# Kernel optimization log

Measured on AMD Instinct MI355X. Metric: run time of the kernel, lower is better.

Reference implementation:

```python
import jax, jax.numpy as jnp
import numpy as np

B, T, E, H = 4, 1024, 1024, 16
D = E // H  # head_dim = 64


def setup_inputs() -> dict:
    key = jax.random.key(0)
    ks = jax.random.split(key, 6)
    s = 0.02  # realistic init scale for stable softmax
    return {
        "hidden_states": jax.random.normal(ks[0], (B, T, E), jnp.float32),
        "attention_mask": jnp.zeros((B, 1, T, T), jnp.float32),
        "Wq": jax.random.normal(ks[1], (E, E), jnp.float32) * s,
        "bq": jnp.zeros((E,), jnp.float32),
        "Wk": jax.random.normal(ks[2], (E, E), jnp.float32) * s,
        "bk": jnp.zeros((E,), jnp.float32),
        "Wv": jax.random.normal(ks[3], (E, E), jnp.float32) * s,
        "bv": jnp.zeros((E,), jnp.float32),
        "Wo": jax.random.normal(ks[4], (E, E), jnp.float32) * s,
        "bo": jnp.zeros((E,), jnp.float32),
    }


def reference(hidden_states, attention_mask, Wq, bq, Wk, bk, Wv, bv, Wo, bo):
    b, t, e = hidden_states.shape
    scaling = jnp.asarray(D, hidden_states.dtype) ** -0.5
    # q_proj weights/bias are pre-scaled in the module; equivalent to scaling q output
    q = (hidden_states @ Wq.T + bq) * scaling      # [B,T,E]
    k = hidden_states @ Wk.T + bk                   # self-attention path (no cache)
    v = hidden_states @ Wv.T + bv
    q = q.reshape(b, t, H, D)
    k = k.reshape(b, t, H, D)
    v = v.reshape(b, t, H, D)
    # bmm(q, k^T): [B,H,T,S] score matrix (materialized, as in the original)
    scores = jnp.einsum("bthd,bshd->bhts", q, k) + attention_mask
    probs = jax.nn.softmax(scores, axis=-1)
    ctx = jnp.einsum("bhts,bshd->bthd", probs, v).reshape(b, t, e)
    return ctx @ Wo.T + bo
```

## Files before the change

kernel.cpp:

```cpp
#include <hip/hip_runtime.h>
#include <math.h>

#define BB 4
#define TT 1024
#define EE 1024
#define HH 16
#define DD 64
#define KDIM 1024
#define N_HS (4096 * 1024)
#define N_W  (1024 * 1024)
#define NQKV (BB * HH * TT * DD)
#define LOG2E 1.44269504088896340736f

typedef _Float16 f16x8 __attribute__((ext_vector_type(8)));
typedef _Float16 f16x4 __attribute__((ext_vector_type(4)));
typedef _Float16 f16x2 __attribute__((ext_vector_type(2)));
typedef float    f32x4 __attribute__((ext_vector_type(4)));

__device__ __forceinline__ unsigned short f2h(float x) {
    _Float16 h = (_Float16)x;
    return __builtin_bit_cast(unsigned short, h);
}
__device__ __forceinline__ void split_h(float x, unsigned short& hi, unsigned short& lo) {
    _Float16 h = (_Float16)x;
    hi = __builtin_bit_cast(unsigned short, h);
    lo = f2h(x - (float)h);
}

__device__ __forceinline__ f16x2 cvt_pk(float a, float b) {
    return __builtin_bit_cast(f16x2, __builtin_amdgcn_cvt_pkrtz(a, b));
}

__device__ __forceinline__ void gload16(const void* g, void* l) {
    __builtin_amdgcn_global_load_lds(
        (const __attribute__((address_space(1))) void*)g,
        (__attribute__((address_space(3))) void*)l, 16, 0, 0);
}

__device__ __forceinline__ float mx3(float a, float b, float c) {
    return fmaxf(fmaxf(a, b), c);
}

__global__ __launch_bounds__(256)
void split_kernel(const float* __restrict__ hs,
                  const float* __restrict__ Wq, const float* __restrict__ Wk,
                  const float* __restrict__ Wv, const float* __restrict__ Wo,
                  const float* __restrict__ mask, int* __restrict__ mflag,
                  unsigned short* __restrict__ ws)
{
    const int u = blockIdx.x * 256 + threadIdx.x;
    if (u < (N_HS / 4) + N_W) {
        const float* src;
        unsigned short* dst;
        if (u < (N_HS / 4)) {
            src = hs + (size_t)u * 4;
            dst = ws + (size_t)u * 4;
        } else {
            int v = u - N_HS / 4;
            int wsel = v >> 18;
            int wo   = v & 0x3FFFF;
            const float* Wsrc = (wsel == 0) ? Wq : (wsel == 1) ? Wk : (wsel == 2) ? Wv : Wo;
            src = Wsrc + (size_t)wo * 4;
            dst = ws + (size_t)N_HS + (size_t)wsel * N_W + (size_t)wo * 4;
        }
        float4 x = *(const float4*)src;
        ushort4 h4;
        h4.x = f2h(x.x); h4.y = f2h(x.y); h4.z = f2h(x.z); h4.w = f2h(x.w);
        *(ushort4*)dst = h4;
    } else {
        int v = u - ((N_HS / 4) + N_W);
        float4 x = *(const float4*)(mask + (size_t)v * 4);
        bool nz = (x.x != 0.f) || (x.y != 0.f) || (x.z != 0.f) || (x.w != 0.f);
        if (__any(nz) && (threadIdx.x & 63) == 0)
            atomicOr(mflag, 1);
    }
}

__global__ __launch_bounds__(256)
void qkv_kernel(const unsigned short* __restrict__ hsp,
                const unsigned short* __restrict__ wqp,
                const float* __restrict__ bq, const float* __restrict__ bk,
                const float* __restrict__ bv,
                unsigned short* __restrict__ qkvb,
                unsigned short* __restrict__ vtp)
{
    __shared__ unsigned short qbuf[128 * 128];
    unsigned short* Ah = qbuf;
    unsigned short* Bh = qbuf + 4096;
    unsigned short* Ts = qbuf;

    const int widx  = blockIdx.x >> 3;
    const int nbase = (blockIdx.x & 7) * 128;
    const int mbase = blockIdx.y * 128;
    const unsigned short* Wp = wqp + (size_t)widx * N_W;
    const float* bias = (widx == 0) ? bq : (widx == 1) ? bk : bv;
    unsigned short* dst = qkvb + (size_t)widx * NQKV;
    const float scale = (widx == 0) ? 0.125f * LOG2E : 1.0f;

    const int tid  = threadIdx.x;
    const int w    = tid >> 6;
    const int lane = tid & 63;
    const int quad = lane >> 4;
    const int l16  = lane & 15;
    const int wm   = (w >> 1) * 64;
    const int wn   = (w & 1) * 64;

    f32x4 acc[4][4];
#pragma unroll
    for (int i = 0; i < 4; i++)
#pragma unroll
        for (int j = 0; j < 4; j++) acc[i][j] = (f32x4)0.f;

#pragma unroll 1
    for (int kt = 0; kt < KDIM; kt += 32) {
        __syncthreads();
#pragma unroll
        for (int i = 0; i < 2; i++) {
            int u = tid + i * 256;
            int r = u >> 2, c = u & 3;
            int q = c ^ ((r >> 1) & 3);
            gload16(hsp + (size_t)(mbase + r) * KDIM + kt + q * 8, &Ah[u * 8]);
            gload16(Wp  + (size_t)(nbase + r) * KDIM + kt + q * 8, &Bh[u * 8]);
        }
        __syncthreads();

        f16x8 af[4], bfr[4];
#pragma unroll
        for (int i = 0; i < 4; i++) {
            int r = wm + i * 16 + l16;
            af[i] = *(const f16x8*)&Ah[(r * 4 + (quad ^ ((r >> 1) & 3))) * 8];
        }
#pragma unroll
        for (int j = 0; j < 4; j++) {
            int r = wn + j * 16 + l16;
            bfr[j] = *(const f16x8*)&Bh[(r * 4 + (quad ^ ((r >> 1) & 3))) * 8];
        }
#pragma unroll
        for (int i = 0; i < 4; i++)
#pragma unroll
            for (int j = 0; j < 4; j++)
                acc[i][j] = __builtin_amdgcn_mfma_f32_16x16x32_f16(af[i], bfr[j], acc[i][j], 0, 0, 0);
    }

    if (widx == 2) {
        __syncthreads();
#pragma unroll
        for (int j = 0; j < 4; j++) {
            int n = wn + j * 16 + l16;
            float bj = bias[nbase + n];
            int x = (n & 15) << 2;
#pragma unroll
            for (int i = 0; i < 4; i++) {
                int t4 = wm + i * 16 + quad * 4;
                ushort4 vw;
                vw.x = f2h(acc[i][j][0] + bj);
                vw.y = f2h(acc[i][j][1] + bj);
                vw.z = f2h(acc[i][j][2] + bj);
                vw.w = f2h(acc[i][j][3] + bj);
                *(ushort4*)&Ts[n * 128 + (t4 ^ x)] = vw;
            }
        }
        __syncthreads();
        const int b  = mbase >> 10;
        const int tb = mbase & 1023;
#pragma unroll
        for (int e = 0; e < 8; e++) {
            int c  = tid + e * 256;
            int n  = c >> 4, ch = c & 15;
            int x  = (n & 15) << 2;
            int s  = ch * 8;
            uint2 a0 = *(const uint2*)&Ts[n * 128 + (s ^ x)];
            uint2 a1 = *(const uint2*)&Ts[n * 128 + ((s + 4) ^ x)];
            int nn = nbase + n;
            int h = nn >> 6, d = nn & 63;
            uint4 o;
            o.x = a0.x; o.y = a0.y; o.z = a1.x; o.w = a1.y;
            *(uint4*)(vtp + (((size_t)(b * HH + h) * DD + d) * TT + tb + s)) = o;
        }
    } else {
#pragma unroll
        for (int j = 0; j < 4; j++) {
            int n = nbase + wn + j * 16 + l16;
            int h = n >> 6, d = n & 63;
            float bj = bias[n];
#pragma unroll
            for (int i = 0; i < 4; i++)
#pragma unroll
                for (int rr = 0; rr < 4; rr++) {
                    int m = mbase + wm + i * 16 + quad * 4 + rr;
                    int b = m >> 10, t = m & 1023;
                    dst[(((size_t)(b * HH + h) * TT + t) * DD + d)] =
                        f2h((acc[i][j][rr] + bj) * scale);
                }
        }
    }
}

__global__ __launch_bounds__(256)
void outproj_kernel(const unsigned short* __restrict__ ctxh,
                    const unsigned short* __restrict__ ctxl,
                    const unsigned short* __restrict__ wop,
                    const float* __restrict__ bo, float* __restrict__ out)
{
    __shared__ unsigned short Ach[64 * 32], Acl[64 * 32], Bh[128 * 32];

    const int nbase = blockIdx.x * 128;
    const int mbase = blockIdx.y * 64;

    const int tid  = threadIdx.x;
    const int w    = tid >> 6;
    const int lane = tid & 63;
    const int quad = lane >> 4;
    const int l16  = lane & 15;
    const int wm   = (w >> 1) * 32;
    const int wn   = (w & 1) * 64;

    f32x4 acc[2][4];
#pragma unroll
    for (int i = 0; i < 2; i++)
#pragma unroll
        for (int j = 0; j < 4; j++) acc[i][j] = (f32x4)0.f;

#pragma unroll 1
    for (int kt = 0; kt < KDIM; kt += 32) {
        __syncthreads();
        {
            int r = tid >> 2, c = tid & 3;
            int q = c ^ ((r >> 1) & 3);
            size_t ga = (size_t)(mbase + r) * KDIM + kt + q * 8;
            gload16(ctxh + ga, &Ach[tid * 8]);
            gload16(ctxl + ga, &Acl[tid * 8]);
        }
#pragma unroll
        for (int i = 0; i < 2; i++) {
            int u = tid + i * 256;
            int r = u >> 2, c = u & 3;
            int q = c ^ ((r >> 1) & 3);
            gload16(wop + (size_t)(nbase + r) * KDIM + kt + q * 8, &Bh[u * 8]);
        }
        __syncthreads();

        f16x8 ah[2], al[2], bfr[4];
#pragma unroll
        for (int i = 0; i < 2; i++) {
            int r = wm + i * 16 + l16;
            int slot = (r * 4 + (quad ^ ((r >> 1) & 3))) * 8;
            ah[i] = *(const f16x8*)&Ach[slot];
            al[i] = *(const f16x8*)&Acl[slot];
        }
#pragma unroll
        for (int j = 0; j < 4; j++) {
            int r = wn + j * 16 + l16;
            bfr[j] = *(const f16x8*)&Bh[(r * 4 + (quad ^ ((r >> 1) & 3))) * 8];
        }
#pragma unroll
        for (int i = 0; i < 2; i++)
#pragma unroll
            for (int j = 0; j < 4; j++) {
                acc[i][j] = __builtin_amdgcn_mfma_f32_16x16x32_f16(ah[i], bfr[j], acc[i][j], 0, 0, 0);
                acc[i][j] = __builtin_amdgcn_mfma_f32_16x16x32_f16(al[i], bfr[j], acc[i][j], 0, 0, 0);
            }
    }

#pragma unroll
    for (int j = 0; j < 4; j++) {
        int n = nbase + wn + j * 16 + l16;
        float bj = bo[n];
#pragma unroll
        for (int i = 0; i < 2; i++)
#pragma unroll
            for (int rr = 0; rr < 4; rr++) {
                int m = mbase + wm + i * 16 + quad * 4 + rr;
                out[(size_t)m * EE + n] = acc[i][j][rr] + bj;
            }
    }
}

__global__ __launch_bounds__(256)
void attn_kernel(const unsigned short* __restrict__ qp_, const unsigned short* __restrict__ kp_,
                 const unsigned short* __restrict__ vtp_,
                 const float* __restrict__ mask, const int* __restrict__ mflag,
                 unsigned short* __restrict__ ctxh, unsigned short* __restrict__ ctxl)
{
    __shared__ unsigned short Ks[2][64 * 64];
    __shared__ unsigned short Vt[2][64 * 64];

    const int bh = blockIdx.y;
    const int b  = bh >> 4;
    const int h  = bh & 15;
    const int m0 = blockIdx.x * 128;
    const size_t hoff = (size_t)bh * TT * DD;
    const unsigned short* qhp = qp_ + hoff;
    const unsigned short* khp = kp_ + hoff;
    const unsigned short* vtp = vtp_ + hoff;
    const float* mb = mask + (size_t)b * TT * TT;

    const int tid  = threadIdx.x;
    const int w    = tid >> 6;
    const int lane = tid & 63;
    const int quad = lane >> 4;
    const int l16  = lane & 15;
    const int mw   = m0 + w * 32;

    const int usemask = mflag[0];

    const int lm7 = l16 & 7;
    const int x0  = l16 * 64 + ((quad)     ^ lm7) * 8;
    const int x1  = l16 * 64 + ((4 + quad) ^ lm7) * 8;
    const int qh  = quad >> 1, ql = quad & 1;
    int yy[4];
#pragma unroll
    for (int t = 0; t < 4; t++)
        yy[t] = l16 * 64 + ((2 * t + qh) ^ lm7) * 8 + ql * 4;
    const unsigned short* Ksf = &Ks[0][0];
    const unsigned short* Vtf = &Vt[0][0];

    f16x8 qf[2][2];
#pragma unroll
    for (int g = 0; g < 2; g++)
#pragma unroll
        for (int s = 0; s < 2; s++)
            qf[g][s] = *(const f16x8*)(qhp + (size_t)(mw + g * 16 + l16) * DD + s * 32 + quad * 8);

    f32x4 o2[2][4];
#pragma unroll
    for (int g = 0; g < 2; g++)
#pragma unroll
        for (int u = 0; u < 4; u++) o2[g][u] = (f32x4)0.f;
    f32x4 lv[2];
    lv[0] = (f32x4)0.f; lv[1] = (f32x4)0.f;
    const f32x4 zc = (f32x4)0.f;
    f16x4 onesv;
    onesv[0] = (_Float16)1.f; onesv[1] = (_Float16)1.f;
    onesv[2] = (_Float16)1.f; onesv[3] = (_Float16)1.f;
    float m_i[2] = { -INFINITY, -INFINITY };

#pragma unroll
    for (int i = 0; i < 2; i++) {
        int u = tid + i * 256;
        int r = u >> 3, cp = u & 7;
        int c = cp ^ (r & 7);
        gload16(khp + (size_t)r * DD + c * 8, &Ks[0][u * 8]);
        gload16(vtp + (size_t)r * TT + c * 8, &Vt[0][u * 8]);
    }
    __syncthreads();

#pragma unroll 2
    for (int it = 0; it < 16; ++it) {
        const int n0  = it * 64;
        const int cur = it & 1;

        if (it < 15) {
#pragma unroll
            for (int i = 0; i < 2; i++) {
                int u = tid + i * 256;
                int r = u >> 3, cp = u & 7;
                int c = cp ^ (r & 7);
                gload16(khp + (size_t)(n0 + 64 + r) * DD + c * 8, &Ks[cur ^ 1][u * 8]);
                gload16(vtp + (size_t)r * TT + n0 + 64 + c * 8,   &Vt[cur ^ 1][u * 8]);
            }
        }

        f32x4 st[2][4];
        if (usemask) {
#pragma unroll
            for (int g = 0; g < 2; g++)
#pragma unroll
                for (int t = 0; t < 4; t++)
#pragma unroll
                    for (int r = 0; r < 4; r++)
                        st[g][t][r] = mb[(size_t)(mw + g * 16 + l16) * TT + n0 + 16 * t + quad * 4 + r] * LOG2E;
        } else {
#pragma unroll
            for (int g = 0; g < 2; g++)
#pragma unroll
                for (int t = 0; t < 4; t++) st[g][t] = zc;
        }

        __builtin_amdgcn_s_setprio(1);
#pragma unroll
        for (int t = 0; t < 4; t++) {
            const f16x8 kf = *(const f16x8*)(Ksf + cur * 4096 + x0 + t * 1024);
            st[0][t] = __builtin_amdgcn_mfma_f32_16x16x32_f16(kf, qf[0][0], st[0][t], 0, 0, 0);
            st[1][t] = __builtin_amdgcn_mfma_f32_16x16x32_f16(kf, qf[1][0], st[1][t], 0, 0, 0);
        }
#pragma unroll
        for (int t = 0; t < 4; t++) {
            const f16x8 kf = *(const f16x8*)(Ksf + cur * 4096 + x1 + t * 1024);
            st[0][t] = __builtin_amdgcn_mfma_f32_16x16x32_f16(kf, qf[0][1], st[0][t], 0, 0, 0);
            st[1][t] = __builtin_amdgcn_mfma_f32_16x16x32_f16(kf, qf[1][1], st[1][t], 0, 0, 0);
        }
        __builtin_amdgcn_s_setprio(0);

        f16x4 pb[2][4];
#pragma unroll
        for (int g = 0; g < 2; g++) {
            float g0 = mx3(st[g][0][0], st[g][0][1], st[g][0][2]);
            float g1 = mx3(st[g][0][3], st[g][1][0], st[g][1][1]);
            float g2 = mx3(st[g][1][2], st[g][1][3], st[g][2][0]);
            float g3 = mx3(st[g][2][1], st[g][2][2], st[g][2][3]);
            float g4 = mx3(st[g][3][0], st[g][3][1], st[g][3][2]);
            float rm = fmaxf(mx3(g0, g1, g2), mx3(g3, g4, st[g][3][3]));
            rm = fmaxf(rm, __shfl_xor(rm, 16));
            rm = fmaxf(rm, __shfl_xor(rm, 32));

            if (__any(rm > m_i[g] + 8.f)) {
                float mn    = fmaxf(m_i[g], rm);
                float alpha = exp2f(m_i[g] - mn);
                m_i[g] = mn;
#pragma unroll
                for (int rr = 0; rr < 4; rr++) lv[g][rr] *= alpha;
#pragma unroll
                for (int u = 0; u < 4; u++)
#pragma unroll
                    for (int rr = 0; rr < 4; rr++) o2[g][u][rr] *= alpha;
            }

#pragma unroll
            for (int t = 0; t < 4; t++) {
                float p0 = exp2f(st[g][t][0] - m_i[g]);
                float p1 = exp2f(st[g][t][1] - m_i[g]);
                float p2 = exp2f(st[g][t][2] - m_i[g]);
                float p3 = exp2f(st[g][t][3] - m_i[g]);
                f16x2 plo = cvt_pk(p0, p1);
                f16x2 phi = cvt_pk(p2, p3);
                f16x4 pv;
                pv[0] = plo[0]; pv[1] = plo[1]; pv[2] = phi[0]; pv[3] = phi[1];
                pb[g][t] = pv;
            }
        }

        __builtin_amdgcn_s_setprio(1);
#pragma unroll
        for (int t = 0; t < 4; t++) {
            lv[0] = __builtin_amdgcn_mfma_f32_16x16x16f16(onesv, pb[0][t], lv[0], 0, 0, 0);
            lv[1] = __builtin_amdgcn_mfma_f32_16x16x16f16(onesv, pb[1][t], lv[1], 0, 0, 0);
        }
#pragma unroll
        for (int u = 0; u < 4; u++) {
#pragma unroll
            for (int t = 0; t < 4; t++) {
                const f16x4 vv = *(const f16x4*)(Vtf + cur * 4096 + yy[t] + u * 1024);
                o2[0][u] = __builtin_amdgcn_mfma_f32_16x16x16f16(vv, pb[0][t], o2[0][u], 0, 0, 0);
                o2[1][u] = __builtin_amdgcn_mfma_f32_16x16x16f16(vv, pb[1][t], o2[1][u], 0, 0, 0);
            }
        }
        __builtin_amdgcn_s_setprio(0);

        __syncthreads();
    }

#pragma unroll
    for (int g = 0; g < 2; g++) {
        float inv = 1.0f / lv[g][0];
        int m = mw + g * 16 + l16;
#pragma unroll
        for (int u = 0; u < 4; u++)
#pragma unroll
            for (int rr = 0; rr < 4; rr++) {
                float val = o2[g][u][rr] * inv;
                unsigned short hi, lo;
                split_h(val, hi, lo);
                size_t off = ((size_t)(b * TT + m)) * EE + h * DD + u * 16 + quad * 4 + rr;
                ctxh[off] = hi;
                ctxl[off] = lo;
            }
    }
}

extern "C" void kernel_launch(void* const* d_in, const int* in_sizes, int n_in,
                              void* d_out, int out_size, void* d_ws, size_t ws_size,
                              hipStream_t stream)
{
    const float* hs   = (const float*)d_in[0];
    const float* mask = (const float*)d_in[1];
    const float* Wq   = (const float*)d_in[2];
    const float* bq   = (const float*)d_in[3];
    const float* Wk   = (const float*)d_in[4];
    const float* bk   = (const float*)d_in[5];
    const float* Wv   = (const float*)d_in[6];
    const float* bv   = (const float*)d_in[7];
    const float* Wo   = (const float*)d_in[8];
    const float* bo   = (const float*)d_in[9];
    float* out = (float*)d_out;

    unsigned short* ws   = (unsigned short*)d_ws;
    unsigned short* hsp  = ws;
    unsigned short* wqp  = ws + (size_t)N_HS;
    unsigned short* wop  = wqp + 3 * (size_t)N_W;
    unsigned short* qkvb = wqp + 4 * (size_t)N_W;
    unsigned short* qp   = qkvb;
    unsigned short* kp   = qp + (size_t)NQKV;
    unsigned short* ctxh = ws;
    unsigned short* ctxl = qkvb + 3 * (size_t)NQKV;
    unsigned short* vtp  = ctxl + (size_t)N_HS;
    int*            mflag = (int*)(vtp + (size_t)NQKV);

    (void)hipMemsetAsync(mflag, 0, sizeof(int), stream);
    split_kernel<<<12288, 256, 0, stream>>>(hs, Wq, Wk, Wv, Wo, mask, mflag, ws);
    qkv_kernel<<<dim3(24, 32), 256, 0, stream>>>(hsp, wqp, bq, bk, bv, qkvb, vtp);
    attn_kernel<<<dim3(TT / 128, BB * HH), 256, 0, stream>>>(qp, kp, vtp, mask, mflag, ctxh, ctxl);
    outproj_kernel<<<dim3(8, 64), 256, 0, stream>>>(ctxh, ctxl, wop, bo, out);
}
```

Before: 233.3 us.

## Deepen GEMM K-tiles to 64 and move V transpose into separate kernel

The QKV and output-projection GEMMs now stage 64-wide K slices per iteration instead of 32, using a new XOR swizzle over 8 chunks. This halves the number of barrier-separated load phases and doubles MFMA work per sync. The V-transpose epilogue is removed from the QKV kernel, so V is written in plain head layout like Q and K, and a new small kernel transposes it afterwards. The trade-off is larger LDS per block, which may lower occupancy, plus an extra launch and an extra read and write pass over V.

Result: faster. 217.7 us (-6.7%).

```diff
diff --git a/kernel.cpp b/kernel.cpp
--- a/kernel.cpp
+++ b/kernel.cpp
@@ -81,13 +81,9 @@
                 const unsigned short* __restrict__ wqp,
                 const float* __restrict__ bq, const float* __restrict__ bk,
                 const float* __restrict__ bv,
-                unsigned short* __restrict__ qkvb,
-                unsigned short* __restrict__ vtp)
+                unsigned short* __restrict__ qkvb)
 {
-    __shared__ unsigned short qbuf[128 * 128];
-    unsigned short* Ah = qbuf;
-    unsigned short* Bh = qbuf + 4096;
-    unsigned short* Ts = qbuf;
+    __shared__ unsigned short Ah[128 * 64], Bh[128 * 64];
 
     const int widx  = blockIdx.x >> 3;
     const int nbase = (blockIdx.x & 7) * 128;
@@ -112,87 +108,87 @@
         for (int j = 0; j < 4; j++) acc[i][j] = (f32x4)0.f;
 
 #pragma unroll 1
-    for (int kt = 0; kt < KDIM; kt += 32) {
+    for (int kt = 0; kt < KDIM; kt += 64) {
         __syncthreads();
 #pragma unroll
-        for (int i = 0; i < 2; i++) {
+        for (int i = 0; i < 4; i++) {
             int u = tid + i * 256;
-            int r = u >> 2, c = u & 3;
-            int q = c ^ ((r >> 1) & 3);
-            gload16(hsp + (size_t)(mbase + r) * KDIM + kt + q * 8, &Ah[u * 8]);
-            gload16(Wp  + (size_t)(nbase + r) * KDIM + kt + q * 8, &Bh[u * 8]);
+            int r = u >> 3, cp = u & 7;
+            int c = cp ^ (r & 7);
+            gload16(hsp + (size_t)(mbase + r) * KDIM + kt + c * 8, &Ah[u * 8]);
+            gload16(Wp  + (size_t)(nbase + r) * KDIM + kt + c * 8, &Bh[u * 8]);
         }
         __syncthreads();
 
-        f16x8 af[4], bfr[4];
-#pragma unroll
-        for (int i = 0; i < 4; i++) {
-            int r = wm + i * 16 + l16;
-            af[i] = *(const f16x8*)&Ah[(r * 4 + (quad ^ ((r >> 1) & 3))) * 8];
-        }
-#pragma unroll
-        for (int j = 0; j < 4; j++) {
-            int r = wn + j * 16 + l16;
-            bfr[j] = *(const f16x8*)&Bh[(r * 4 + (quad ^ ((r >> 1) & 3))) * 8];
-        }
+#pragma unroll
+        for (int ks = 0; ks < 2; ks++) {
+            f16x8 af[4], bfr[4];
+#pragma unroll
+            for (int i = 0; i < 4; i++) {
+                int r = wm + i * 16 + l16;
+                af[i] = *(const f16x8*)&Ah[(r * 8 + ((ks * 4 + quad) ^ (r & 7))) * 8];
+            }
+#pragma unroll
+            for (int j = 0; j < 4; j++) {
+                int r = wn + j * 16 + l16;
+                bfr[j] = *(const f16x8*)&Bh[(r * 8 + ((ks * 4 + quad) ^ (r & 7))) * 8];
+            }
+#pragma unroll
+            for (int i = 0; i < 4; i++)
+#pragma unroll
+                for (int j = 0; j < 4; j++)
+                    acc[i][j] = __builtin_amdgcn_mfma_f32_16x16x32_f16(af[i], bfr[j], acc[i][j], 0, 0, 0);
+        }
+    }
+
+#pragma unroll
+    for (int j = 0; j < 4; j++) {
+        int n = nbase + wn + j * 16 + l16;
+        int h = n >> 6, d = n & 63;
+        float bj = bias[n];
 #pragma unroll
         for (int i = 0; i < 4; i++)
 #pragma unroll
-            for (int j = 0; j < 4; j++)
-                acc[i][j] = __builtin_amdgcn_mfma_f32_16x16x32_f16(af[i], bfr[j], acc[i][j], 0, 0, 0);
-    }
-
-    if (widx == 2) {
-        __syncthreads();
-#pragma unroll
-        for (int j = 0; j < 4; j++) {
-            int n = wn + j * 16 + l16;
-            float bj = bias[nbase + n];
-            int x = (n & 15) << 2;
-#pragma unroll
-            for (int i = 0; i < 4; i++) {
-                int t4 = wm + i * 16 + quad * 4;
-                ushort4 vw;
-                vw.x = f2h(acc[i][j][0] + bj);
-                vw.y = f2h(acc[i][j][1] + bj);
-                vw.z = f2h(acc[i][j][2] + bj);
-                vw.w = f2h(acc[i][j][3] + bj);
-                *(ushort4*)&Ts[n * 128 + (t4 ^ x)] = vw;
-            }
-        }
-        __syncthreads();
-        const int b  = mbase >> 10;
-        const int tb = mbase & 1023;
-#pragma unroll
-        for (int e = 0; e < 8; e++) {
-            int c  = tid + e * 256;
-            int n  = c >> 4, ch = c & 15;
-            int x  = (n & 15) << 2;
-            int s  = ch * 8;
-            uint2 a0 = *(const uint2*)&Ts[n * 128 + (s ^ x)];
-            uint2 a1 = *(const uint2*)&Ts[n * 128 + ((s + 4) ^ x)];
-            int nn = nbase + n;
-            int h = nn >> 6, d = nn & 63;
-            uint4 o;
-            o.x = a0.x; o.y = a0.y; o.z = a1.x; o.w = a1.y;
-            *(uint4*)(vtp + (((size_t)(b * HH + h) * DD + d) * TT + tb + s)) = o;
-        }
-    } else {
-#pragma unroll
-        for (int j = 0; j < 4; j++) {
-            int n = nbase + wn + j * 16 + l16;
-            int h = n >> 6, d = n & 63;
-            float bj = bias[n];
-#pragma unroll
-            for (int i = 0; i < 4; i++)
-#pragma unroll
-                for (int rr = 0; rr < 4; rr++) {
-                    int m = mbase + wm + i * 16 + quad * 4 + rr;
-                    int b = m >> 10, t = m & 1023;
-                    dst[(((size_t)(b * HH + h) * TT + t) * DD + d)] =
-                        f2h((acc[i][j][rr] + bj) * scale);
-                }
-        }
+            for (int rr = 0; rr < 4; rr++) {
+                int m = mbase + wm + i * 16 + quad * 4 + rr;
+                int b = m >> 10, t = m & 1023;
+                dst[(((size_t)(b * HH + h) * TT + t) * DD + d)] =
+                    f2h((acc[i][j][rr] + bj) * scale);
+            }
+    }
+}
+
+__global__ __launch_bounds__(256)
+void vtrans_kernel(const unsigned short* __restrict__ vp,
+                   unsigned short* __restrict__ vtp)
+{
+    __shared__ unsigned short Ts[64 * 72];
+    const int bh = blockIdx.y;
+    const int t0 = blockIdx.x * 64;
+    const unsigned short* src = vp  + (size_t)bh * TT * DD + (size_t)t0 * DD;
+    unsigned short*       dst = vtp + (size_t)bh * DD * TT + t0;
+    const int tid = threadIdx.x;
+
+#pragma unroll
+    for (int i = 0; i < 2; i++) {
+        int id = tid + i * 256;
+        int r = id >> 3, c = id & 7;
+        *(uint4*)&Ts[r * 72 + c * 8] = *(const uint4*)(src + (size_t)r * DD + c * 8);
+    }
+    __syncthreads();
+#pragma unroll
+    for (int i = 0; i < 2; i++) {
+        int id = tid + i * 256;
+        int d = id >> 3, c = id & 7;
+        unsigned short tmp[8];
+#pragma unroll
+        for (int j = 0; j < 8; j++) tmp[j] = Ts[(c * 8 + j) * 72 + d];
+        uint4 o;
+        o.x = (unsigned int)tmp[0] | ((unsigned int)tmp[1] << 16);
+        o.y = (unsigned int)tmp[2] | ((unsigned int)tmp[3] << 16);
+        o.z = (unsigned int)tmp[4] | ((unsigned int)tmp[5] << 16);
+        o.w = (unsigned int)tmp[6] | ((unsigned int)tmp[7] << 16);
+        *(uint4*)(dst + (size_t)d * TT + c * 8) = o;
     }
 }
 
@@ -202,7 +198,7 @@
                     const unsigned short* __restrict__ wop,
                     const float* __restrict__ bo, float* __restrict__ out)
 {
-    __shared__ unsigned short Ach[64 * 32], Acl[64 * 32], Bh[128 * 32];
+    __shared__ unsigned short Ach[64 * 64], Acl[64 * 64], Bh[128 * 64];
 
     const int nbase = blockIdx.x * 128;
     const int mbase = blockIdx.y * 64;
@@ -222,44 +218,49 @@
         for (int j = 0; j < 4; j++) acc[i][j] = (f32x4)0.f;
 
 #pragma unroll 1
-    for (int kt = 0; kt < KDIM; kt += 32) {
+    for (int kt = 0; kt < KDIM; kt += 64) {
         __syncthreads();
-        {
-            int r = tid >> 2, c = tid & 3;
-            int q = c ^ ((r >> 1) & 3);
-            size_t ga = (size_t)(mbase + r) * KDIM + kt + q * 8;
-            gload16(ctxh + ga, &Ach[tid * 8]);
-            gload16(ctxl + ga, &Acl[tid * 8]);
-        }
 #pragma unroll
         for (int i = 0; i < 2; i++) {
             int u = tid + i * 256;
-            int r = u >> 2, c = u & 3;
-            int q = c ^ ((r >> 1) & 3);
-            gload16(wop + (size_t)(nbase + r) * KDIM + kt + q * 8, &Bh[u * 8]);
+            int r = u >> 3, cp = u & 7;
+            int c = cp ^ (r & 7);
+            size_t ga = (size_t)(mbase + r) * KDIM + kt + c * 8;
+            gload16(ctxh + ga, &Ach[u * 8]);
+            gload16(ctxl + ga, &Acl[u * 8]);
+        }
+#pragma unroll
+        for (int i = 0; i < 4; i++) {
+            int u = tid + i * 256;
+            int r = u >> 3, cp = u & 7;
+            int c = cp ^ (r & 7);
+            gload16(wop + (size_t)(nbase + r) * KDIM + kt + c * 8, &Bh[u * 8]);
         }
         __syncthreads();
 
-        f16x8 ah[2], al[2], bfr[4];
-#pragma unroll
-        for (int i = 0; i < 2; i++) {
-            int r = wm + i * 16 + l16;
-            int slot = (r * 4 + (quad ^ ((r >> 1) & 3))) * 8;
-            ah[i] = *(const f16x8*)&Ach[slot];
-            al[i] = *(const f16x8*)&Acl[slot];
-        }
-#pragma unroll
-        for (int j = 0; j < 4; j++) {
-            int r = wn + j * 16 + l16;
-            bfr[j] = *(const f16x8*)&Bh[(r * 4 + (quad ^ ((r >> 1) & 3))) * 8];
-        }
-#pragma unroll
-        for (int i = 0; i < 2; i++)
+#pragma unroll
+        for (int ks = 0; ks < 2; ks++) {
+            f16x8 ah[2], al[2], bfr[4];
+#pragma unroll
+            for (int i = 0; i < 2; i++) {
+                int r = wm + i * 16 + l16;
+                int slot = (r * 8 + ((ks * 4 + quad) ^ (r & 7))) * 8;
+                ah[i] = *(const f16x8*)&Ach[slot];
+                al[i] = *(const f16x8*)&Acl[slot];
+            }
 #pragma unroll
             for (int j = 0; j < 4; j++) {
-                acc[i][j] = __builtin_amdgcn_mfma_f32_16x16x32_f16(ah[i], bfr[j], acc[i][j], 0, 0, 0);
-                acc[i][j] = __builtin_amdgcn_mfma_f32_16x16x32_f16(al[i], bfr[j], acc[i][j], 0, 0, 0);
-            }
+                int r = wn + j * 16 + l16;
+                bfr[j] = *(const f16x8*)&Bh[(r * 8 + ((ks * 4 + quad) ^ (r & 7))) * 8];
+            }
+#pragma unroll
+            for (int i = 0; i < 2; i++)
+#pragma unroll
+                for (int j = 0; j < 4; j++) {
+                    acc[i][j] = __builtin_amdgcn_mfma_f32_16x16x32_f16(ah[i], bfr[j], acc[i][j], 0, 0, 0);
+                    acc[i][j] = __builtin_amdgcn_mfma_f32_16x16x32_f16(al[i], bfr[j], acc[i][j], 0, 0, 0);
+                }
+        }
     }
 
 #pragma unroll
@@ -491,6 +492,7 @@
     unsigned short* qkvb = wqp + 4 * (size_t)N_W;
     unsigned short* qp   = qkvb;
     unsigned short* kp   = qp + (size_t)NQKV;
+    unsigned short* vp   = kp + (size_t)NQKV;
     unsigned short* ctxh = ws;
     unsigned short* ctxl = qkvb + 3 * (size_t)NQKV;
     unsigned short* vtp  = ctxl + (size_t)N_HS;
@@ -498,7 +500,8 @@
 
     (void)hipMemsetAsync(mflag, 0, sizeof(int), stream);
     split_kernel<<<12288, 256, 0, stream>>>(hs, Wq, Wk, Wv, Wo, mask, mflag, ws);
-    qkv_kernel<<<dim3(24, 32), 256, 0, stream>>>(hsp, wqp, bq, bk, bv, qkvb, vtp);
+    qkv_kernel<<<dim3(24, 32), 256, 0, stream>>>(hsp, wqp, bq, bk, bv, qkvb);
+    vtrans_kernel<<<dim3(TT / 64, BB * HH), 256, 0, stream>>>(vp, vtp);
     attn_kernel<<<dim3(TT / 128, BB * HH), 256, 0, stream>>>(qp, kp, vtp, mask, mflag, ctxh, ctxl);
     outproj_kernel<<<dim3(8, 64), 256, 0, stream>>>(ctxh, ctxl, wop, bo, out);
 }
```
